# Optimization experiments

Measured on AMD Instinct MI355X. Metric: run time of the kernel, lower is better.

## Reference

```python
import jax, jax.numpy as jnp
import numpy as np

D_MODEL = 1024
NEG_INF = -1000000000.0


def setup_inputs() -> dict:
    key = jax.random.key(0)
    ks = jax.random.split(key, 9)
    B, S, D = 8, 2048, D_MODEL
    scale = 1.0 / np.sqrt(D)
    return {
        "x": jax.random.normal(ks[0], (B, S, D), dtype=jnp.float32),
        "mask": jax.random.randint(ks[1], (B, S), 0, 2, dtype=jnp.int32),
        "Wq": jax.random.normal(ks[2], (D, D), dtype=jnp.float32) * scale,
        "bq": jnp.zeros((D,), dtype=jnp.float32),
        "Wk": jax.random.normal(ks[3], (D, D), dtype=jnp.float32) * scale,
        "bk": jnp.zeros((D,), dtype=jnp.float32),
        "Wv": jax.random.normal(ks[4], (D, D), dtype=jnp.float32) * scale,
        "bv": jnp.zeros((D,), dtype=jnp.float32),
    }


def reference(x, mask, Wq, bq, Wk, bk, Wv, bv):
    # QKV projections (torch Linear: x @ W^T + b)
    q = jnp.einsum("bsd,ed->bse", x, Wq) + bq
    k = jnp.einsum("bsd,ed->bse", x, Wk) + bk
    v = jnp.einsum("bsd,ed->bse", x, Wv) + bv
    d = q.shape[-1]
    scores = jnp.einsum("bqd,bkd->bqk", q, k) / jnp.sqrt(jnp.float32(d))
    # mask [B, S] broadcast over query dim; masked_fill where mask == 0
    scores = jnp.where(mask[:, None, :] == 0, NEG_INF, scores)
    p_attn = jax.nn.softmax(scores, axis=-1)
    # dropout is identity in eval/reference mode
    return jnp.einsum("bqk,bkd->bqd", p_attn, v)
```

## Files before the change

kernel.cpp:

```cpp
#include <hip/hip_runtime.h>
#include <hip/hip_bf16.h>
#include <hip/hip_fp16.h>

#define NEG_INF -1000000000.0f

typedef __attribute__((ext_vector_type(8))) short bf16x8;
typedef __attribute__((ext_vector_type(4))) float f32x4;

__device__ __forceinline__ unsigned short f2bf(float f) {
    unsigned int u = __float_as_uint(f);
    u += 0x7FFFu + ((u >> 16) & 1u);
    return (unsigned short)(u >> 16);
}

__device__ __forceinline__ float h2f(unsigned short us) {
    __half h;
    __builtin_memcpy(&h, &us, 2);
    return __half2float(h);
}

#define GLOAD_LDS16(gp, lp)                                                  \
    __builtin_amdgcn_global_load_lds(                                        \
        (const __attribute__((address_space(1))) void*)(gp),                 \
        (__attribute__((address_space(3))) void*)(lp), 16, 0, 0)

template<int EPI>
__global__ __launch_bounds__(512, 2)
void gemm256(const unsigned short* __restrict__ A, const unsigned short* __restrict__ B,
             void* __restrict__ C0, void* __restrict__ C1, void* __restrict__ C2,
             const float* __restrict__ b0, const float* __restrict__ b1,
             const float* __restrict__ b2,
             int K, long lda, long ldb, long ldc,
             long batchA, long batchB, long batchC,
             int gx, int gy)
{
    __shared__ unsigned short As[2][16384];
    __shared__ unsigned short Bs[2][16384];

    int bid = blockIdx.x;
    bid = (bid & 7) * ((int)gridDim.x >> 3) + (bid >> 3);
    const int gxy = gx * gy;
    const int bz  = bid / gxy;
    const int rem = bid - bz * gxy;
    const int tm  = rem / gy;
    const int bm  = tm * 256;
    const int bn  = (rem - tm * gy) * 256;

    const int t    = threadIdx.x;
    const int lane = t & 63;
    const int w    = t >> 6;
    const int wr   = w >> 2;
    const int wc   = w & 3;
    const int lr   = lane & 15;
    const int lkg  = lane >> 4;
    const int sx8  = (lr & 7) * 8;
    const int e0   = (lkg * 8) ^ sx8;

    const int tr  = t >> 3;
    const int tcs = ((t & 7) ^ (tr & 7)) * 8;
    const int wb512 = w * 512;

    const unsigned short* Ab = A + (size_t)bz * (size_t)batchA + (size_t)(bm + tr) * lda + tcs;
    const unsigned short* Bb = B + (size_t)bz * (size_t)batchB + (size_t)(bn + tr) * ldb + tcs;

#define ST_A(nb, L, kt) GLOAD_LDS16(Ab + (size_t)(L) * 64 * lda + (kt), &As[nb][(L) * 4096 + wb512])
#define ST_B(nb, L, kt) GLOAD_LDS16(Bb + (size_t)(L) * 64 * ldb + (kt), &Bs[nb][(L) * 4096 + wb512])

    f32x4 acc[8][4];
#pragma unroll
    for (int i = 0; i < 8; ++i)
#pragma unroll
        for (int j = 0; j < 4; ++j)
            acc[i][j] = f32x4{0.f, 0.f, 0.f, 0.f};

    ST_B(0, 0, 0); ST_B(0, 1, 0); ST_B(0, 2, 0); ST_B(0, 3, 0);
    ST_A(0, 0, 0); ST_A(0, 2, 0); ST_A(0, 1, 0); ST_A(0, 3, 0);
    asm volatile("s_waitcnt vmcnt(2)" ::: "memory");
    __builtin_amdgcn_s_barrier();

    bf16x8 a[2][2], b[4][2];

#define READ_B(BUF)                                                          \
    _Pragma("unroll") for (int j = 0; j < 4; ++j) {                          \
        const int Rb = wc * 64 + j * 16 + lr;                                \
        b[j][0] = *(const bf16x8*)&Bs[BUF][Rb * 64 + e0];                    \
        b[j][1] = *(const bf16x8*)&Bs[BUF][Rb * 64 + (e0 ^ 32)];             \
    }

#define LOAD_A(BUF, qp)                                                      \
    _Pragma("unroll") for (int i2 = 0; i2 < 2; ++i2) {                       \
        const int Ra = wr * 128 + (qp) * 32 + i2 * 16 + lr;                  \
        a[i2][0] = *(const bf16x8*)&As[BUF][Ra * 64 + e0];                   \
        a[i2][1] = *(const bf16x8*)&As[BUF][Ra * 64 + (e0 ^ 32)];            \
    }

#define MFMA_Q(qp)                                                           \
    __builtin_amdgcn_s_setprio(1);                                           \
    _Pragma("unroll") for (int kk = 0; kk < 2; ++kk)                         \
    _Pragma("unroll") for (int i2 = 0; i2 < 2; ++i2)                         \
    _Pragma("unroll") for (int j = 0; j < 4; ++j)                            \
        acc[(qp) * 2 + i2][j] = __builtin_amdgcn_mfma_f32_16x16x32_bf16(     \
            a[i2][kk], b[j][kk], acc[(qp) * 2 + i2][j], 0, 0, 0);            \
    __builtin_amdgcn_s_setprio(0);

#define TILE(BUF, STAGE, ktn)                                                \
    {                                                                        \
        const int buf_ = (BUF); const int nb_ = buf_ ^ 1;                    \
          \
        READ_B(buf_)                                                         \
        LOAD_A(buf_, 0)                                                      \
        if (STAGE) { ST_B(nb_, 0, ktn); ST_B(nb_, 1, ktn); }                 \
        __builtin_amdgcn_s_barrier();                                        \
        MFMA_Q(0)                                                            \
        __builtin_amdgcn_s_barrier();                                        \
                                                                \
        LOAD_A(buf_, 1)                                                      \
        if (STAGE) { ST_B(nb_, 2, ktn); ST_B(nb_, 3, ktn); }                 \
        __builtin_amdgcn_s_barrier();                                        \
        MFMA_Q(1)                                                            \
        if (STAGE) { asm volatile("s_waitcnt vmcnt(4)" ::: "memory"); }      \
        else       { asm volatile("s_waitcnt vmcnt(0)" ::: "memory"); }      \
        __builtin_amdgcn_s_barrier();                                        \
                                                                \
        LOAD_A(buf_, 2)                                                      \
        if (STAGE) { ST_A(nb_, 0, ktn); ST_A(nb_, 2, ktn); }                 \
        __builtin_amdgcn_s_barrier();                                        \
        MFMA_Q(2)                                                            \
        __builtin_amdgcn_s_barrier();                                        \
                                                                \
        LOAD_A(buf_, 3)                                                      \
        if (STAGE) { ST_A(nb_, 1, ktn); ST_A(nb_, 3, ktn); }                 \
        __builtin_amdgcn_s_barrier();                                        \
        MFMA_Q(3)                                                            \
        if (STAGE) { asm volatile("s_waitcnt vmcnt(2)" ::: "memory"); }      \
        __builtin_amdgcn_s_barrier();                                        \
    }

    const int NT = K >> 6;
    for (int k = 0; k < NT - 1; ++k) {
        TILE(k & 1, true, (k + 1) << 6);
    }
    TILE((NT - 1) & 1, false, 0);

#undef TILE
#undef MFMA_Q
#undef LOAD_A
#undef READ_B
#undef ST_A
#undef ST_B

    const int r0 = lkg * 4;
    const size_t coff = (size_t)bz * (size_t)batchC;
#pragma unroll
    for (int ri = 0; ri < 8; ++ri) {
#pragma unroll
        for (int j = 0; j < 4; ++j) {
            if (EPI == 0) {
                const int which = bn >> 10;
                const float scl = (which == 0) ? 0.03125f : 1.0f;
                const float* bias = (which == 0) ? b0 : (which == 1 ? b1 : b2);
                unsigned short* dst = (unsigned short*)
                    ((which == 0) ? C0 : (which == 1 ? C1 : C2));
                const int gcol3 = bn + wc * 64 + j * 16 + lr;
                const int col   = gcol3 & 1023;
                const float bv  = bias[col];
                if (which == 2) {
                    const int m0 = bm + wr * 128 + ri * 16 + r0;
                    const int bb = m0 >> 11;
                    const int s0 = m0 & 2047;
                    ushort4 wv;
                    wv.x = f2bf(acc[ri][j][0] + bv);
                    wv.y = f2bf(acc[ri][j][1] + bv);
                    wv.z = f2bf(acc[ri][j][2] + bv);
                    wv.w = f2bf(acc[ri][j][3] + bv);
                    *(ushort4*)(dst + (size_t)bb * (1024 * 2048)
                                + (size_t)col * 2048 + s0) = wv;
                } else {
#pragma unroll
                    for (int r = 0; r < 4; ++r) {
                        const int grow = bm + wr * 128 + ri * 16 + r0 + r;
                        dst[(size_t)grow * ldc + col] = f2bf((acc[ri][j][r] + bv) * scl);
                    }
                }
            } else if (EPI == 1) {
                const int gcol = bn + wc * 64 + j * 16 + lr;
#pragma unroll
                for (int r = 0; r < 4; ++r) {
                    const int grow = bm + wr * 128 + ri * 16 + r0 + r;
                    ((__half*)C0)[coff + (size_t)grow * ldc + gcol] =
                        __float2half(acc[ri][j][r]);
                }
            } else {
                const int gcol = bn + wc * 64 + j * 16 + lr;
#pragma unroll
                for (int r = 0; r < 4; ++r) {
                    const int grow = bm + wr * 128 + ri * 16 + r0 + r;
                    ((float*)C0)[coff + (size_t)grow * ldc + gcol] = acc[ri][j][r];
                }
            }
        }
    }
}

__global__ __launch_bounds__(256)
void conv_f32_bf16(const float4* __restrict__ src, ushort4* __restrict__ dst, int n4)
{
    const int i = blockIdx.x * 256 + threadIdx.x;
    if (i < n4) {
        const float4 v = src[i];
        ushort4 wv;
        wv.x = f2bf(v.x); wv.y = f2bf(v.y); wv.z = f2bf(v.z); wv.w = f2bf(v.w);
        dst[i] = wv;
    }
}

__global__ __launch_bounds__(256)
void softmax_rows(const __half* __restrict__ S, const int* __restrict__ mask,
                  unsigned short* __restrict__ P)
{
    const size_t row = blockIdx.x;
    const int b = (int)(row >> 11);
    const __half* sr = S + row * 2048;
    unsigned short* pr = P + row * 2048;
    const int t = threadIdx.x;

    const ushort4 h0 = *(const ushort4*)&sr[t * 8];
    const ushort4 h1 = *(const ushort4*)&sr[t * 8 + 4];
    const int4 mv0 = *(const int4*)&mask[b * 2048 + t * 8];
    const int4 mv1 = *(const int4*)&mask[b * 2048 + t * 8 + 4];

    float s[8];
    s[0] = h2f(h0.x); s[1] = h2f(h0.y); s[2] = h2f(h0.z); s[3] = h2f(h0.w);
    s[4] = h2f(h1.x); s[5] = h2f(h1.y); s[6] = h2f(h1.z); s[7] = h2f(h1.w);
    if (mv0.x == 0) s[0] = NEG_INF;
    if (mv0.y == 0) s[1] = NEG_INF;
    if (mv0.z == 0) s[2] = NEG_INF;
    if (mv0.w == 0) s[3] = NEG_INF;
    if (mv1.x == 0) s[4] = NEG_INF;
    if (mv1.y == 0) s[5] = NEG_INF;
    if (mv1.z == 0) s[6] = NEG_INF;
    if (mv1.w == 0) s[7] = NEG_INF;

    float m = fmaxf(fmaxf(fmaxf(s[0], s[1]), fmaxf(s[2], s[3])),
                    fmaxf(fmaxf(s[4], s[5]), fmaxf(s[6], s[7])));

    __shared__ float red[256];
    red[t] = m;
    __syncthreads();
    for (int sw = 128; sw > 0; sw >>= 1) {
        if (t < sw) red[t] = fmaxf(red[t], red[t + sw]);
        __syncthreads();
    }
    const float mx = red[0];
    __syncthreads();

    float e[8];
#pragma unroll
    for (int j = 0; j < 8; ++j) e[j] = __expf(s[j] - mx);
    float s8 = ((e[0] + e[1]) + (e[2] + e[3])) + ((e[4] + e[5]) + (e[6] + e[7]));

    red[t] = s8;
    __syncthreads();
    for (int sw = 128; sw > 0; sw >>= 1) {
        if (t < sw) red[t] += red[t + sw];
        __syncthreads();
    }
    const float inv = 1.0f / red[0];

    ushort4 w0, w1;
    w0.x = f2bf(e[0] * inv); w0.y = f2bf(e[1] * inv);
    w0.z = f2bf(e[2] * inv); w0.w = f2bf(e[3] * inv);
    w1.x = f2bf(e[4] * inv); w1.y = f2bf(e[5] * inv);
    w1.z = f2bf(e[6] * inv); w1.w = f2bf(e[7] * inv);
    *(ushort4*)&pr[t * 8]     = w0;
    *(ushort4*)&pr[t * 8 + 4] = w1;
}

extern "C" void kernel_launch(void* const* d_in, const int* in_sizes, int n_in,
                              void* d_out, int out_size, void* d_ws, size_t ws_size,
                              hipStream_t stream)
{
    const float* x    = (const float*)d_in[0];
    const int*   mask = (const int*)d_in[1];
    const float* Wq   = (const float*)d_in[2];
    const float* bq   = (const float*)d_in[3];
    const float* Wk   = (const float*)d_in[4];
    const float* bk   = (const float*)d_in[5];
    const float* Wv   = (const float*)d_in[6];
    const float* bv   = (const float*)d_in[7];
    float* out = (float*)d_out;

    char* ws = (char*)d_ws;
    unsigned short* Q  = (unsigned short*)(ws);
    unsigned short* Kt = (unsigned short*)(ws + (32ull << 20));
    unsigned short* Vt = (unsigned short*)(ws + (64ull << 20));
    __half*         Sf = (__half*)(ws + (96ull << 20));
    unsigned short* P  = (unsigned short*)(ws + (160ull << 20));
    unsigned short* xb = (unsigned short*)(ws + (160ull << 20));
    unsigned short* wb = (unsigned short*)(ws + (192ull << 20));

    const int D = 1024, S = 2048, B = 8, Mtot = 16384;
    dim3 blk2(256), blk5(512);

    conv_f32_bf16<<<dim3((Mtot * D / 4) / 256), blk2, 0, stream>>>((const float4*)x, (ushort4*)xb, Mtot * D / 4);
    conv_f32_bf16<<<dim3((D * D / 4) / 256), blk2, 0, stream>>>((const float4*)Wq, (ushort4*)(wb + 0ull * D * D), D * D / 4);
    conv_f32_bf16<<<dim3((D * D / 4) / 256), blk2, 0, stream>>>((const float4*)Wk, (ushort4*)(wb + 1ull * D * D), D * D / 4);
    conv_f32_bf16<<<dim3((D * D / 4) / 256), blk2, 0, stream>>>((const float4*)Wv, (ushort4*)(wb + 2ull * D * D), D * D / 4);

    gemm256<0><<<dim3(768), blk5, 0, stream>>>(
        xb, wb, Q, Kt, Vt, bq, bk, bv,
        D, 1024, 1024, 1024, 0, 0, 0, 64, 12);

    gemm256<1><<<dim3(512), blk5, 0, stream>>>(
        Q, Kt, Sf, nullptr, nullptr, nullptr, nullptr, nullptr,
        D, 1024, 1024, 2048, (long)S * D, (long)S * D, (long)S * S, 8, 8);

    softmax_rows<<<dim3(B * S), blk2, 0, stream>>>(Sf, mask, P);

    gemm256<2><<<dim3(256), blk5, 0, stream>>>(
        P, Vt, out, nullptr, nullptr, nullptr, nullptr, nullptr,
        S, 2048, 2048, 1024, (long)S * 2048, (long)D * S, (long)S * D, 8, 4);
}
```

Measured before the change: 299.9 us.

## Compact unmasked keys to skip masked columns in K/V, QK^T and PV GEMMs

After: 266.3 us. 1.13x faster.

```diff
diff --git a/kernel.cpp b/kernel.cpp
--- a/kernel.cpp
+++ b/kernel.cpp
@@ -27,9 +27,9 @@
 template<int EPI>
 __global__ __launch_bounds__(512, 2)
 void gemm256(const unsigned short* __restrict__ A, const unsigned short* __restrict__ B,
-             void* __restrict__ C0, void* __restrict__ C1, void* __restrict__ C2,
+             void* __restrict__ C0, void* __restrict__ C1,
              const float* __restrict__ b0, const float* __restrict__ b1,
-             const float* __restrict__ b2,
+             const int* __restrict__ cidx, const int* __restrict__ ncinfo,
              int K, long lda, long ldb, long ldc,
              long batchA, long batchB, long batchC,
              int gx, int gy)
@@ -45,6 +45,9 @@
     const int tm  = rem / gy;
     const int bm  = tm * 256;
     const int bn  = (rem - tm * gy) * 256;
+
+    if (EPI == 3) { if (bm >= ncinfo[8 + bz]) return; }
+    if (EPI == 1) { if (bn >= ncinfo[8 + bz]) return; }
 
     const int t    = threadIdx.x;
     const int lane = t & 63;
@@ -63,7 +66,20 @@
     const unsigned short* Ab = A + (size_t)bz * (size_t)batchA + (size_t)(bm + tr) * lda + tcs;
     const unsigned short* Bb = B + (size_t)bz * (size_t)batchB + (size_t)(bn + tr) * ldb + tcs;
 
-#define ST_A(nb, L, kt) GLOAD_LDS16(Ab + (size_t)(L) * 64 * lda + (kt), &As[nb][(L) * 4096 + wb512])
+    const unsigned short* ApG[4];
+#pragma unroll
+    for (int L = 0; L < 4; ++L) {
+        if (EPI == 3) {
+            const int rr = cidx[bz * 2048 + bm + L * 64 + tr];
+            ApG[L] = A + ((size_t)bz * 2048 + rr) * lda + tcs;
+        } else {
+            ApG[L] = Ab + (size_t)L * 64 * lda;
+        }
+    }
+
+    const int Kd = (EPI == 2) ? ncinfo[8 + bz] : K;
+
+#define ST_A(nb, L, kt) GLOAD_LDS16(ApG[L] + (kt), &As[nb][(L) * 4096 + wb512])
 #define ST_B(nb, L, kt) GLOAD_LDS16(Bb + (size_t)(L) * 64 * ldb + (kt), &Bs[nb][(L) * 4096 + wb512])
 
     f32x4 acc[8][4];
@@ -136,7 +152,7 @@
         __builtin_amdgcn_s_barrier();                                        \
     }
 
-    const int NT = K >> 6;
+    const int NT = Kd >> 6;
     for (int k = 0; k < NT - 1; ++k) {
         TILE(k & 1, true, (k + 1) << 6);
     }
@@ -156,31 +172,35 @@
 #pragma unroll
         for (int j = 0; j < 4; ++j) {
             if (EPI == 0) {
-                const int which = bn >> 10;
-                const float scl = (which == 0) ? 0.03125f : 1.0f;
-                const float* bias = (which == 0) ? b0 : (which == 1 ? b1 : b2);
-                unsigned short* dst = (unsigned short*)
-                    ((which == 0) ? C0 : (which == 1 ? C1 : C2));
+                const int gcol = bn + wc * 64 + j * 16 + lr;
+                const float bv = b0[gcol];
+#pragma unroll
+                for (int r = 0; r < 4; ++r) {
+                    const int grow = bm + wr * 128 + ri * 16 + r0 + r;
+                    ((unsigned short*)C0)[(size_t)grow * ldc + gcol] =
+                        f2bf((acc[ri][j][r] + bv) * 0.03125f);
+                }
+            } else if (EPI == 3) {
                 const int gcol3 = bn + wc * 64 + j * 16 + lr;
+                const int which = gcol3 >> 10;
                 const int col   = gcol3 & 1023;
-                const float bv  = bias[col];
-                if (which == 2) {
+                const float bv  = (which == 0) ? b0[col] : b1[col];
+                if (which == 0) {
+                    unsigned short* dst = (unsigned short*)C0 + (size_t)bz * (2048 * 1024);
+#pragma unroll
+                    for (int r = 0; r < 4; ++r) {
+                        const int grow = bm + wr * 128 + ri * 16 + r0 + r;
+                        dst[(size_t)grow * 1024 + col] = f2bf(acc[ri][j][r] + bv);
+                    }
+                } else {
                     const int m0 = bm + wr * 128 + ri * 16 + r0;
-                    const int bb = m0 >> 11;
-                    const int s0 = m0 & 2047;
                     ushort4 wv;
                     wv.x = f2bf(acc[ri][j][0] + bv);
                     wv.y = f2bf(acc[ri][j][1] + bv);
                     wv.z = f2bf(acc[ri][j][2] + bv);
                     wv.w = f2bf(acc[ri][j][3] + bv);
-                    *(ushort4*)(dst + (size_t)bb * (1024 * 2048)
-                                + (size_t)col * 2048 + s0) = wv;
-                } else {
-#pragma unroll
-                    for (int r = 0; r < 4; ++r) {
-                        const int grow = bm + wr * 128 + ri * 16 + r0 + r;
-                        dst[(size_t)grow * ldc + col] = f2bf((acc[ri][j][r] + bv) * scl);
-                    }
+                    *(ushort4*)((unsigned short*)C1 + (size_t)bz * (1024 * 2048)
+                                + (size_t)col * 2048 + m0) = wv;
                 }
             } else if (EPI == 1) {
                 const int gcol = bn + wc * 64 + j * 16 + lr;
@@ -215,31 +235,62 @@
 }
 
 __global__ __launch_bounds__(256)
-void softmax_rows(const __half* __restrict__ S, const int* __restrict__ mask,
-                  unsigned short* __restrict__ P)
+void compact_mask(const int* __restrict__ mask, int* __restrict__ cidx,
+                  int* __restrict__ ncinfo)
+{
+    const int b = blockIdx.x;
+    const int t = threadIdx.x;
+    const int* mb = mask + b * 2048;
+    int loc[8];
+    int c = 0;
+#pragma unroll
+    for (int j = 0; j < 8; ++j) {
+        const int s = t * 8 + j;
+        if (mb[s] != 0) loc[c++] = s;
+    }
+    __shared__ int ps[256];
+    ps[t] = c;
+    __syncthreads();
+    for (int off = 1; off < 256; off <<= 1) {
+        const int v = (t >= off) ? ps[t - off] : 0;
+        __syncthreads();
+        ps[t] += v;
+        __syncthreads();
+    }
+    const int base = ps[t] - c;
+    int* cb = cidx + b * 2048;
+    for (int i = 0; i < c; ++i) cb[base + i] = loc[i];
+    __syncthreads();
+    const int nc  = ps[255];
+    int ncp = (nc + 255) & ~255;
+    if (ncp < 256) ncp = 256;
+    for (int i = nc + t; i < ncp; i += 256) cb[i] = 0;
+    if (t == 0) { ncinfo[b] = nc; ncinfo[8 + b] = ncp; }
+}
+
+__global__ __launch_bounds__(256)
+void softmax_rows(unsigned short* __restrict__ SP, const int* __restrict__ ncinfo)
 {
     const size_t row = blockIdx.x;
-    const int b = (int)(row >> 11);
-    const __half* sr = S + row * 2048;
-    unsigned short* pr = P + row * 2048;
-    const int t = threadIdx.x;
-
-    const ushort4 h0 = *(const ushort4*)&sr[t * 8];
-    const ushort4 h1 = *(const ushort4*)&sr[t * 8 + 4];
-    const int4 mv0 = *(const int4*)&mask[b * 2048 + t * 8];
-    const int4 mv1 = *(const int4*)&mask[b * 2048 + t * 8 + 4];
+    const int b   = (int)(row >> 11);
+    const int nc  = ncinfo[b];
+    const int ncp = ncinfo[8 + b];
+    unsigned short* sp = SP + row * 2048;
+    const int t  = threadIdx.x;
+    const int c0 = t * 8;
+    const bool act = c0 < ncp;
 
     float s[8];
-    s[0] = h2f(h0.x); s[1] = h2f(h0.y); s[2] = h2f(h0.z); s[3] = h2f(h0.w);
-    s[4] = h2f(h1.x); s[5] = h2f(h1.y); s[6] = h2f(h1.z); s[7] = h2f(h1.w);
-    if (mv0.x == 0) s[0] = NEG_INF;
-    if (mv0.y == 0) s[1] = NEG_INF;
-    if (mv0.z == 0) s[2] = NEG_INF;
-    if (mv0.w == 0) s[3] = NEG_INF;
-    if (mv1.x == 0) s[4] = NEG_INF;
-    if (mv1.y == 0) s[5] = NEG_INF;
-    if (mv1.z == 0) s[6] = NEG_INF;
-    if (mv1.w == 0) s[7] = NEG_INF;
+#pragma unroll
+    for (int j = 0; j < 8; ++j) s[j] = NEG_INF;
+    if (act) {
+        const ushort4 h0 = *(const ushort4*)&sp[c0];
+        const ushort4 h1 = *(const ushort4*)&sp[c0 + 4];
+        const unsigned short hv[8] = {h0.x, h0.y, h0.z, h0.w, h1.x, h1.y, h1.z, h1.w};
+#pragma unroll
+        for (int j = 0; j < 8; ++j)
+            if (c0 + j < nc) s[j] = h2f(hv[j]);
+    }
 
     float m = fmaxf(fmaxf(fmaxf(s[0], s[1]), fmaxf(s[2], s[3])),
                     fmaxf(fmaxf(s[4], s[5]), fmaxf(s[6], s[7])));
@@ -267,13 +318,15 @@
     }
     const float inv = 1.0f / red[0];
 
-    ushort4 w0, w1;
-    w0.x = f2bf(e[0] * inv); w0.y = f2bf(e[1] * inv);
-    w0.z = f2bf(e[2] * inv); w0.w = f2bf(e[3] * inv);
-    w1.x = f2bf(e[4] * inv); w1.y = f2bf(e[5] * inv);
-    w1.z = f2bf(e[6] * inv); w1.w = f2bf(e[7] * inv);
-    *(ushort4*)&pr[t * 8]     = w0;
-    *(ushort4*)&pr[t * 8 + 4] = w1;
+    if (act) {
+        ushort4 w0, w1;
+        w0.x = f2bf(e[0] * inv); w0.y = f2bf(e[1] * inv);
+        w0.z = f2bf(e[2] * inv); w0.w = f2bf(e[3] * inv);
+        w1.x = f2bf(e[4] * inv); w1.y = f2bf(e[5] * inv);
+        w1.z = f2bf(e[6] * inv); w1.w = f2bf(e[7] * inv);
+        *(ushort4*)&sp[c0]     = w0;
+        *(ushort4*)&sp[c0 + 4] = w1;
+    }
 }
 
 extern "C" void kernel_launch(void* const* d_in, const int* in_sizes, int n_in,
@@ -291,13 +344,14 @@
     float* out = (float*)d_out;
 
     char* ws = (char*)d_ws;
-    unsigned short* Q  = (unsigned short*)(ws);
-    unsigned short* Kt = (unsigned short*)(ws + (32ull << 20));
-    unsigned short* Vt = (unsigned short*)(ws + (64ull << 20));
-    __half*         Sf = (__half*)(ws + (96ull << 20));
-    unsigned short* P  = (unsigned short*)(ws + (160ull << 20));
-    unsigned short* xb = (unsigned short*)(ws + (160ull << 20));
-    unsigned short* wb = (unsigned short*)(ws + (192ull << 20));
+    unsigned short* Q   = (unsigned short*)(ws);
+    unsigned short* Kc  = (unsigned short*)(ws + (32ull << 20));
+    unsigned short* Vtc = (unsigned short*)(ws + (64ull << 20));
+    unsigned short* SP  = (unsigned short*)(ws + (96ull << 20));
+    unsigned short* xb  = (unsigned short*)(ws + (160ull << 20));
+    unsigned short* wb  = (unsigned short*)(ws + (192ull << 20));
+    int*            cidx   = (int*)(ws + (198ull << 20));
+    int*            ncinfo = (int*)(ws + (199ull << 20));
 
     const int D = 1024, S = 2048, B = 8, Mtot = 16384;
     dim3 blk2(256), blk5(512);
@@ -307,17 +361,23 @@
     conv_f32_bf16<<<dim3((D * D / 4) / 256), blk2, 0, stream>>>((const float4*)Wk, (ushort4*)(wb + 1ull * D * D), D * D / 4);
     conv_f32_bf16<<<dim3((D * D / 4) / 256), blk2, 0, stream>>>((const float4*)Wv, (ushort4*)(wb + 2ull * D * D), D * D / 4);
 
-    gemm256<0><<<dim3(768), blk5, 0, stream>>>(
-        xb, wb, Q, Kt, Vt, bq, bk, bv,
-        D, 1024, 1024, 1024, 0, 0, 0, 64, 12);
+    compact_mask<<<dim3(B), blk2, 0, stream>>>(mask, cidx, ncinfo);
+
+    gemm256<0><<<dim3(256), blk5, 0, stream>>>(
+        xb, wb, Q, nullptr, bq, nullptr, nullptr, nullptr,
+        D, 1024, 1024, 1024, 0, 0, 0, 64, 4);
+
+    gemm256<3><<<dim3(512), blk5, 0, stream>>>(
+        xb, wb + 1ull * D * D, Kc, Vtc, bk, bv, cidx, ncinfo,
+        D, 1024, 1024, 1024, 0, 0, 0, 8, 8);
 
     gemm256<1><<<dim3(512), blk5, 0, stream>>>(
-        Q, Kt, Sf, nullptr, nullptr, nullptr, nullptr, nullptr,
+        Q, Kc, SP, nullptr, nullptr, nullptr, nullptr, ncinfo,
         D, 1024, 1024, 2048, (long)S * D, (long)S * D, (long)S * S, 8, 8);
 
-    softmax_rows<<<dim3(B * S), blk2, 0, stream>>>(Sf, mask, P);
+    softmax_rows<<<dim3(B * S), blk2, 0, stream>>>(SP, ncinfo);
 
     gemm256<2><<<dim3(256), blk5, 0, stream>>>(
-        P, Vt, out, nullptr, nullptr, nullptr, nullptr, nullptr,
+        SP, Vtc, out, nullptr, nullptr, nullptr, nullptr, ncinfo,
         S, 2048, 2048, 1024, (long)S * 2048, (long)D * S, (long)S * D, 8, 4);
 }
```
